# Optimization experiments

Hardware: AMD Instinct MI355X
Metric: run time of the kernel (lower is better)

The kernel has to match this reference:

```python
import jax, jax.numpy as jnp
import numpy as np

RRELU_SLOPE = (1.0 / 8.0 + 1.0 / 3.0) / 2.0  # F.rrelu eval-mode slope
DILATIONS = (1, 2, 4, 8)
HIDDEN_TEMP = 1.0
GUMBEL_TEMP = 0.1


def rrelu(x):
    return jnp.where(x >= 0, x, RRELU_SLOPE * x)


def conv1d(x, w, b, dilation):
    # x: [B, Cin, T], w: [Cout, Cin, K] -> [B, Cout, T'] (VALID, dilated)
    y = jax.lax.conv_general_dilated(
        x, w, window_strides=(1,), padding='VALID', rhs_dilation=(dilation,),
        dimension_numbers=('NCH', 'OIH', 'NCH'))
    return y + b[None, :, None]


def setup_inputs() -> dict:
    key = jax.random.key(0)
    ks = jax.random.split(key, 16)
    B, D, T, R = 8, 32, 4096, 8
    s = 0.05  # param scale for numerical stability
    inp = {
        'x': jax.random.normal(ks[0], (B, D, T), jnp.float32),
        'u': jax.random.uniform(ks[1], (B, T, R), jnp.float32, 1e-6, 1.0 - 1e-6),
        'conv_w0': jax.random.normal(ks[2], (128, D, 2), jnp.float32) * s,
        'conv_b0': jax.random.normal(ks[3], (128,), jnp.float32) * s,
        'conv_w1': jax.random.normal(ks[4], (128, 128, 2), jnp.float32) * s,
        'conv_b1': jax.random.normal(ks[5], (128,), jnp.float32) * s,
        'conv_w2': jax.random.normal(ks[6], (128, 128, 2), jnp.float32) * s,
        'conv_b2': jax.random.normal(ks[7], (128,), jnp.float32) * s,
        'conv_w3': jax.random.normal(ks[8], (R, 128, 2), jnp.float32) * s,
        'conv_b3': jax.random.normal(ks[9], (R,), jnp.float32) * s,
        'pw0': jax.random.normal(ks[10], (R, 256, 128), jnp.float32) * s,
        'pb0': jax.random.normal(ks[11], (R, 256), jnp.float32) * s,
        'pw1': jax.random.normal(ks[12], (R, 2 * D, 256), jnp.float32) * s,
        'pb1': jax.random.normal(ks[13], (R, 2 * D), jnp.float32) * s,
    }
    return inp


def reference(x, u, conv_w0, conv_b0, conv_w1, conv_b1, conv_w2, conv_b2,
              conv_w3, conv_b3, pw0, pb0, pw1, pb1):
    pad = sum(DILATIONS)  # causal left pad
    h = jnp.pad(x, ((0, 0), (0, 0), (pad, 0)))
    for w, b, d in ((conv_w0, conv_b0, DILATIONS[0]),
                    (conv_w1, conv_b1, DILATIONS[1]),
                    (conv_w2, conv_b2, DILATIONS[2])):
        h = rrelu(conv1d(h, w, b, d))
    pre = h  # [B, 128, T + dilations[-1]]
    h_vecs = rrelu(conv1d(pre, conv_w3, conv_b3, DILATIONS[3]))  # [B, R, T]
    pre = pre[:, :, DILATIONS[3]:]  # [B, 128, T]

    p = jax.nn.softmax(h_vecs / HIDDEN_TEMP, axis=1)  # [B, R, T]
    logits = jnp.log(p).transpose(0, 2, 1)  # [B, T, R]
    g = -jnp.log(-jnp.log(u))  # gumbel noise from uniform input
    gen_z = jax.nn.softmax((logits + g) / GUMBEL_TEMP, axis=-1).transpose(0, 2, 1)  # [B, R, T]

    # Fused mixture-of-experts dynamic linear: equal to materializing
    # einsum('brt,roi->boit') then contracting with pre, but avoids the huge tensor.
    params = (jnp.einsum('brt,roi,bit->bot', gen_z, pw0, pre)
              + jnp.einsum('brt,ro->bot', gen_z, pb0))
    # NOTE: original calls F.rrelu(params) without assignment -> no-op (kept faithful)
    params = (jnp.einsum('brt,roi,bit->bot', gen_z, pw1, params)
              + jnp.einsum('brt,ro->bot', gen_z, pb1))

    mus, sig = jnp.split(params, 2, axis=1)  # each [B, n_dims, T]
    sigmas = 0.5 + 0.5 * jnp.tanh(sig) + 0.001
    return mus, sigmas, gen_z
```

## Files before the change

### kernel.cpp

```cpp
#include <hip/hip_runtime.h>
#include <math.h>

typedef __attribute__((ext_vector_type(8))) short bf16x8;
typedef __attribute__((ext_vector_type(4))) float f32x4;
struct __align__(8)  us4 { unsigned short x,y,z,w; };
struct __align__(16) ui4 { unsigned x,y,z,w; };

#define SLOPE 0.2291666666666667f
constexpr int N0=4110, N1=4108, N2=4104, NX=4111;

__device__ __forceinline__ unsigned short f2bf(float f){
  unsigned u = __float_as_uint(f);
  u = (u + 0x7FFF + ((u>>16)&1)) >> 16;
  return (unsigned short)u;
}
__device__ __forceinline__ float bf2f(unsigned short h){
  return __uint_as_float(((unsigned)h)<<16);
}
__device__ __forceinline__ float rrelu(float v){ return v>=0.f ? v : v*SLOPE; }

__global__ __launch_bounds__(256) void prep_w(
  const float* __restrict__ w0, const float* __restrict__ w1, const float* __restrict__ w2,
  const float* __restrict__ pw0, const float* __restrict__ pw1,
  const float* __restrict__ pb0, const float* __restrict__ pb1,
  unsigned short* __restrict__ w0e, unsigned short* __restrict__ w1e, unsigned short* __restrict__ w2e,
  unsigned short* __restrict__ pw0b, unsigned short* __restrict__ pw1b,
  unsigned short* __restrict__ pb0e, unsigned short* __restrict__ pb1e)
{
  int idx = blockIdx.x*256 + threadIdx.x;
  if (idx < 8192){ int oc=idx>>6, k=idx&63, tap=k>>5, i=k&31;
    w0e[idx] = f2bf(w0[(oc*32+i)*2+tap]); return; }
  idx -= 8192;
  if (idx < 32768){ int oc=idx>>8, k=idx&255, tap=k>>7, i=k&127;
    w1e[idx] = f2bf(w1[(oc*128+i)*2+tap]); return; }
  idx -= 32768;
  if (idx < 32768){ int oc=idx>>8, k=idx&255, tap=k>>7, i=k&127;
    w2e[idx] = f2bf(w2[(oc*128+i)*2+tap]); return; }
  idx -= 32768;
  if (idx < 262144){ pw0b[idx] = f2bf(pw0[idx]); return; }
  idx -= 262144;
  if (idx < 131072){ pw1b[idx] = f2bf(pw1[idx]); return; }
  idx -= 131072;
  if (idx < 8192){ int o=idx>>5, r=idx&31; pb0e[idx] = r<8 ? f2bf(pb0[r*256+o]) : (unsigned short)0; return; }
  idx -= 8192;
  if (idx < 2048){ int o=idx>>5, r=idx&31; pb1e[idx] = r<8 ? f2bf(pb1[r*64+o]) : (unsigned short)0; return; }
}

__global__ __launch_bounds__(64) void prep_xt(const float* __restrict__ x,
                                              unsigned short* __restrict__ xt)
{
  __shared__ float s[32][64];
  const int b = blockIdx.y, j0 = blockIdx.x*64, l = threadIdx.x;
  #pragma unroll 4
  for (int i=0;i<32;i++){
    int p = j0 + l - 15;
    s[i][l] = (p>=0 && p<4096) ? x[((size_t)b*32+i)*4096+p] : 0.f;
  }
  __syncthreads();
  const int j = j0 + l;
  if (j < NX){
    unsigned tmp[16];
    #pragma unroll
    for (int q=0;q<16;q++)
      tmp[q] = (unsigned)f2bf(s[2*q][l]) | ((unsigned)f2bf(s[2*q+1][l])<<16);
    ui4* dst = (ui4*)(xt + ((size_t)b*NX + j)*32);
    #pragma unroll
    for (int q=0;q<4;q++){ ui4 v={tmp[4*q],tmp[4*q+1],tmp[4*q+2],tmp[4*q+3]}; dst[q]=v; }
  }
}

template<int IC, int DIL, int NIN, int NOUT>
__global__ __launch_bounds__(256) void conv_g(
    const unsigned short* __restrict__ act,
    const unsigned short* __restrict__ wgt,
    const float* __restrict__ bias,
    unsigned short* __restrict__ outp)
{
  constexpr int KT   = 2*IC;
  constexpr int NK   = KT/32;
  constexpr int NH   = (KT > 128) ? 2 : 1;
  constexpr int KPH  = KT / NH;
  constexpr int NKH  = KPH/32;
  constexpr int HRB  = KPH*2;
  constexpr int HCPR = HRB/16;
  __shared__ __align__(16) char wsm[64*HRB];
  __shared__ __align__(16) char outs[64*128];

  const int tid = threadIdx.x;
  const int b = blockIdx.z, ob = blockIdx.y, tb = blockIdx.x*64;
  const int o0g = ob*64;
  const int wid = tid>>6, l = tid&63, lo = l&15, hi = l>>4;

  bf16x8 bfr[NK];
  {
    const int tg = tb + wid*16 + lo;
    const int te = tg < NOUT ? tg : NOUT-1;
    #pragma unroll
    for (int kk=0;kk<NK;kk++){
      int k = kk*32 + hi*8;
      int tap = (k >= IC) ? 1 : 0;
      int off = k - tap*IC;
      bfr[kk] = *(const bf16x8*)(act + ((size_t)b*NIN + te + tap*DIL)*IC + off);
    }
  }

  f32x4 acc[4];
  #pragma unroll
  for (int m=0;m<4;m++) acc[m] = (f32x4){0.f,0.f,0.f,0.f};

  #pragma unroll
  for (int h=0; h<NH; ++h){
    __syncthreads();
    for (int c = tid; c < 64*HCPR; c += 256){
      int row = c / HCPR, cc = c % HCPR;
      ui4 v = *(const ui4*)((const char*)wgt + (size_t)(o0g+row)*KT*2 + h*HRB + cc*16);
      *(ui4*)(wsm + row*HRB + ((cc*16) ^ ((row&7)<<4))) = v;
    }
    __syncthreads();
    #pragma unroll
    for (int kk=0;kk<NKH;kk++){
      #pragma unroll
      for (int m=0;m<4;m++){
        int row = m*16 + lo;
        bf16x8 af = *(const bf16x8*)(wsm + row*HRB + ((kk*64+hi*16) ^ ((row&7)<<4)));
        acc[m] = __builtin_amdgcn_mfma_f32_16x16x32_bf16(af, bfr[h*NKH+kk], acc[m], 0,0,0);
      }
    }
  }
  __syncthreads();
  #pragma unroll
  for (int m=0;m<4;m++){
    const int ol = m*16 + hi*4;
    float b0v = bias[o0g+ol+0], b1v = bias[o0g+ol+1], b2v = bias[o0g+ol+2], b3v = bias[o0g+ol+3];
    int tl = wid*16 + lo;
    us4 v;
    v.x = f2bf(rrelu(acc[m][0] + b0v));
    v.y = f2bf(rrelu(acc[m][1] + b1v));
    v.z = f2bf(rrelu(acc[m][2] + b2v));
    v.w = f2bf(rrelu(acc[m][3] + b3v));
    *(us4*)(outs + tl*128 + ((ol*2) ^ ((tl&7)<<4))) = v;
  }
  __syncthreads();
  #pragma unroll
  for (int i=0;i<2;i++){
    int c = tid + i*256;
    int row = c>>3, cc = c&7;
    if (tb + row < NOUT){
      ui4 v = *(const ui4*)(outs + row*128 + ((cc*16) ^ ((row&7)<<4)));
      *(ui4*)(outp + ((size_t)b*NOUT + tb + row)*128 + o0g + cc*8) = v;
    }
  }
}

__global__ __launch_bounds__(64) void gumbel_g(
  const unsigned short* __restrict__ h2t,
  const float* __restrict__ w3, const float* __restrict__ b3,
  const float* __restrict__ u,
  float* __restrict__ genz,
  unsigned short* __restrict__ zt)
{
  __shared__ unsigned hs[72][66];
  const int b = blockIdx.y, t0 = blockIdx.x*64, l = threadIdx.x;
  const unsigned* src = (const unsigned*)(h2t + ((size_t)b*N2 + t0)*128);
  for (int e=l; e<72*64; e+=64) hs[e>>6][e&63] = src[e];
  __syncthreads();

  float acc[8];
  #pragma unroll
  for (int r=0;r<8;r++) acc[r]=b3[r];
  for (int i2=0;i2<64;i2++){
    unsigned a0 = hs[l][i2], a1 = hs[l+8][i2];
    float v00 = bf2f(a0&0xffff), v01 = bf2f(a0>>16);
    float v10 = bf2f(a1&0xffff), v11 = bf2f(a1>>16);
    const int i = 2*i2;
    #pragma unroll
    for (int r=0;r<8;r++){
      acc[r] = fmaf(w3[(r*128+i)*2],     v00, acc[r]);
      acc[r] = fmaf(w3[(r*128+i)*2+1],   v10, acc[r]);
      acc[r] = fmaf(w3[(r*128+i+1)*2],   v01, acc[r]);
      acc[r] = fmaf(w3[(r*128+i+1)*2+1], v11, acc[r]);
    }
  }
  float m = -1e30f;
  #pragma unroll
  for (int r=0;r<8;r++){ acc[r] = rrelu(acc[r]); m = fmaxf(m, acc[r]); }
  float s = 0.f;
  #pragma unroll
  for (int r=0;r<8;r++) s += __expf(acc[r]-m);
  const float lse = m + __logf(s);
  const int t = t0 + l;
  const float* ub = u + ((size_t)b*4096 + t)*8;
  float y[8], m2 = -1e30f;
  #pragma unroll
  for (int r=0;r<8;r++){
    float g = -__logf(-__logf(ub[r]));
    y[r] = (acc[r] - lse + g)*10.f;
    m2 = fmaxf(m2, y[r]);
  }
  float s2 = 0.f;
  #pragma unroll
  for (int r=0;r<8;r++){ y[r] = __expf(y[r]-m2); s2 += y[r]; }
  const float inv = 1.f/s2;
  #pragma unroll
  for (int r=0;r<8;r++){
    y[r] *= inv;
    genz[((size_t)b*8+r)*4096 + t] = y[r];
  }
  ui4 zp = { (unsigned)f2bf(y[0]) | ((unsigned)f2bf(y[1])<<16),
             (unsigned)f2bf(y[2]) | ((unsigned)f2bf(y[3])<<16),
             (unsigned)f2bf(y[4]) | ((unsigned)f2bf(y[5])<<16),
             (unsigned)f2bf(y[6]) | ((unsigned)f2bf(y[7])<<16) };
  ui4 zz = {0,0,0,0};
  ui4* zd = (ui4*)(zt + ((size_t)b*4096 + t)*32);
  zd[0]=zp; zd[1]=zz; zd[2]=zz; zd[3]=zz;
}

__global__ __launch_bounds__(256) void moe1_m(
  const unsigned short* __restrict__ h2t,
  const float* __restrict__ genz,
  const unsigned short* __restrict__ zt,
  const unsigned short* __restrict__ pw0b,
  const unsigned short* __restrict__ pb0e,
  unsigned short* __restrict__ hidt)
{
  __shared__ __align__(16) char pres[32768];
  __shared__ __align__(16) char outb[16384];
  __shared__ float zl[1024];

  const int ob = blockIdx.x, b = blockIdx.z, tb = blockIdx.y*128;
  const int o0g = ob*64;
  const int tid = threadIdx.x;
  #pragma unroll
  for (int i=0;i<4;i++){
    int e = tid + i*256;
    zl[e] = genz[((size_t)b*8 + (e>>7))*4096 + tb + (e&127)];
  }
  {
    const char* src = (const char*)(h2t + ((size_t)b*N2 + tb + 8)*128);
    #pragma unroll
    for (int i=0;i<8;i++){
      int c = tid + i*256, row = c>>4, cc = c&15;
      ui4 v = *(const ui4*)(src + row*256 + cc*16);
      *(ui4*)(pres + row*256 + ((cc*16) ^ ((row&7)<<4))) = v;
    }
  }
  __syncthreads();

  const int wid = tid>>6, l = tid&63, lo = l&15, hi = l>>4;
  const int ow = o0g + wid*16;

  f32x4 acc[8];
  {
    bf16x8 pf = *(const bf16x8*)(pb0e + (size_t)(ow + lo)*32 + hi*8);
    #pragma unroll
    for (int n=0;n<8;n++){
      bf16x8 zf = *(const bf16x8*)(zt + ((size_t)b*4096 + tb + n*16 + lo)*32 + hi*8);
      acc[n] = __builtin_amdgcn_mfma_f32_16x16x32_bf16(pf, zf, (f32x4){0.f,0.f,0.f,0.f}, 0,0,0);
    }
  }

  const unsigned short* abase = pw0b + (size_t)(ow + lo)*128 + hi*8;
  bf16x8 A[4], An[4];
  #pragma unroll
  for (int kk=0;kk<4;kk++) A[kk] = *(const bf16x8*)(abase + kk*32);

  #pragma unroll
  for (int r=0;r<8;r++){
    if (r < 7){
      #pragma unroll
      for (int kk=0;kk<4;kk++)
        An[kk] = *(const bf16x8*)(abase + (size_t)(r+1)*32768 + kk*32);
    }
    f32x4 ar[8];
    #pragma unroll
    for (int n=0;n<8;n++) ar[n] = (f32x4){0.f,0.f,0.f,0.f};
    #pragma unroll
    for (int kk=0;kk<4;kk++){
      #pragma unroll
      for (int n=0;n<8;n++){
        int tl = n*16 + lo;
        bf16x8 bf = *(const bf16x8*)(pres + tl*256 + ((kk*64 + hi*16) ^ ((tl&7)<<4)));
        ar[n] = __builtin_amdgcn_mfma_f32_16x16x32_bf16(A[kk], bf, ar[n], 0,0,0);
      }
    }
    #pragma unroll
    for (int n=0;n<8;n++){
      float zv = zl[r*128 + n*16 + lo];
      #pragma unroll
      for (int c2=0;c2<4;c2++)
        acc[n][c2] = fmaf(zv, ar[n][c2], acc[n][c2]);
    }
    if (r < 7){
      #pragma unroll
      for (int kk=0;kk<4;kk++) A[kk] = An[kk];
    }
  }

  #pragma unroll
  for (int n=0;n<8;n++){
    int tl = n*16 + lo;
    int ol2 = (wid*16 + hi*4)*2;
    us4 v;
    v.x=f2bf(acc[n][0]); v.y=f2bf(acc[n][1]); v.z=f2bf(acc[n][2]); v.w=f2bf(acc[n][3]);
    *(us4*)(outb + tl*128 + (ol2 ^ ((tl&7)<<4))) = v;
  }
  __syncthreads();
  #pragma unroll
  for (int i=0;i<4;i++){
    int c = tid + i*256, row = c>>3, cc = c&7;
    ui4 v = *(const ui4*)(outb + row*128 + ((cc*16) ^ ((row&7)<<4)));
    *(ui4*)(hidt + (((size_t)b*4 + ob)*4096 + tb + row)*64 + cc*8) = v;
  }
}

__global__ __launch_bounds__(512) void moe2_m(
  const unsigned short* __restrict__ hidt,
  const float* __restrict__ genz,
  const unsigned short* __restrict__ zt,
  const unsigned short* __restrict__ pw1b,
  const unsigned short* __restrict__ pb1e,
  float* __restrict__ out)
{
  __shared__ __align__(16) char smem[32768*2 + 4096];
  char* abuf0 = smem;
  char* abuf1 = smem + 32768;
  float* zl  = (float*)(smem + 65536);

  const int wg = blockIdx.x;
  const int b = wg >> 5, tb = (wg & 31) * 128;

  const int tid = threadIdx.x;
  #pragma unroll
  for (int i=0;i<2;i++){
    int e = tid + i*512;
    zl[e] = genz[((size_t)b*8 + (e>>7))*4096 + tb + (e&127)];
  }

  const int wid = tid>>6, l = tid&63, lo = l&15, hi = l>>4;
  const int tg = tb + wid*16 + lo;

  bf16x8 bfr[8];
  #pragma unroll
  for (int kk=0;kk<8;kk++)
    bfr[kk] = *(const bf16x8*)(hidt + (((size_t)b*4 + (kk>>1))*4096 + tg)*64 + (kk&1)*32 + hi*8);
  f32x4 acc[4];
  {
    bf16x8 zf = *(const bf16x8*)(zt + ((size_t)b*4096 + tg)*32 + hi*8);
    #pragma unroll
    for (int m=0;m<4;m++){
      bf16x8 pf = *(const bf16x8*)(pb1e + (size_t)(m*16 + lo)*32 + hi*8);
      acc[m] = __builtin_amdgcn_mfma_f32_16x16x32_bf16(pf, zf, (f32x4){0.f,0.f,0.f,0.f}, 0,0,0);
    }
  }

  {
    const char* src = (const char*)pw1b;
    #pragma unroll
    for (int i=0;i<4;i++){
      int c = tid + i*512, row = c>>5, cc = c&31;
      ui4 v = *(const ui4*)(src + row*512 + cc*16);
      *(ui4*)(abuf0 + row*512 + ((cc*16) ^ ((row&7)<<4))) = v;
    }
  }
  __syncthreads();

  #pragma unroll
  for (int r=0;r<8;r++){
    char* cur = (r&1) ? abuf1 : abuf0;
    char* nxt = (r&1) ? abuf0 : abuf1;
    ui4 stg[4];
    if (r < 7){
      const char* src = (const char*)(pw1b + (size_t)(r+1)*16384);
      #pragma unroll
      for (int i=0;i<4;i++){
        int c = tid + i*512;
        stg[i] = *(const ui4*)(src + (c>>5)*512 + (c&31)*16);
      }
    }
    f32x4 ar[4];
    #pragma unroll
    for (int m=0;m<4;m++) ar[m] = (f32x4){0.f,0.f,0.f,0.f};
    #pragma unroll
    for (int kk=0;kk<8;kk++){
      #pragma unroll
      for (int m=0;m<4;m++){
        int row = m*16 + lo;
        int kb  = kk*64 + hi*16;
        bf16x8 af = *(const bf16x8*)(cur + row*512 + (kb ^ ((row&7)<<4)));
        ar[m] = __builtin_amdgcn_mfma_f32_16x16x32_bf16(af, bfr[kk], ar[m], 0,0,0);
      }
    }
    float zv = zl[r*128 + wid*16 + lo];
    #pragma unroll
    for (int m=0;m<4;m++)
      #pragma unroll
      for (int c2=0;c2<4;c2++)
        acc[m][c2] = fmaf(zv, ar[m][c2], acc[m][c2]);
    if (r < 7){
      #pragma unroll
      for (int i=0;i<4;i++){
        int c = tid + i*512;
        *(ui4*)(nxt + (c>>5)*512 + (((c&31)*16) ^ (((c>>5)&7)<<4))) = stg[i];
      }
    }
    __syncthreads();
  }

  #pragma unroll
  for (int m=0;m<4;m++){
    #pragma unroll
    for (int c2=0;c2<4;c2++){
      int o = m*16 + hi*4 + c2;
      float v = acc[m][c2];
      if (o < 32)
        out[((size_t)b*32 + o)*4096 + tg] = v;
      else {
        float e = __expf(2.f*v);
        float th = 1.f - 2.f/(e+1.f);
        out[(size_t)1048576 + ((size_t)b*32 + (o-32))*4096 + tg] = 0.5f + 0.5f*th + 0.001f;
      }
    }
  }
}

extern "C" void kernel_launch(void* const* d_in, const int* in_sizes, int n_in,
                              void* d_out, int out_size, void* d_ws, size_t ws_size,
                              hipStream_t stream) {
  const float* x   = (const float*)d_in[0];
  const float* u   = (const float*)d_in[1];
  const float* w0  = (const float*)d_in[2];
  const float* b0  = (const float*)d_in[3];
  const float* w1  = (const float*)d_in[4];
  const float* b1  = (const float*)d_in[5];
  const float* w2  = (const float*)d_in[6];
  const float* b2  = (const float*)d_in[7];
  const float* w3  = (const float*)d_in[8];
  const float* b3  = (const float*)d_in[9];
  const float* pw0 = (const float*)d_in[10];
  const float* pb0 = (const float*)d_in[11];
  const float* pw1 = (const float*)d_in[12];
  const float* pb1 = (const float*)d_in[13];

  float* out  = (float*)d_out;
  float* genz = out + (size_t)2*8*32*4096;

  char* p = (char*)d_ws;
  unsigned short* xt   = (unsigned short*)p; p += 2104832;
  unsigned short* h0t  = (unsigned short*)p; p += 8417280;
  unsigned short* h1t  = (unsigned short*)p; p += 8413184;
  unsigned short* h2t  = (unsigned short*)p; p += 8404992;
  unsigned short* ztb  = (unsigned short*)p; p += 2097152;
  unsigned short* hidt = (unsigned short*)p; p += 16777216;
  unsigned short* w0e  = (unsigned short*)p; p += 16384;
  unsigned short* w1e  = (unsigned short*)p; p += 65536;
  unsigned short* w2e  = (unsigned short*)p; p += 65536;
  unsigned short* pw0b = (unsigned short*)p; p += 524288;
  unsigned short* pw1b = (unsigned short*)p; p += 262144;
  unsigned short* pb0e = (unsigned short*)p; p += 16384;
  unsigned short* pb1e = (unsigned short*)p; p += 4096;

  prep_w<<<1864, 256, 0, stream>>>(w0,w1,w2,pw0,pw1,pb0,pb1,
                                   w0e,w1e,w2e,pw0b,pw1b,pb0e,pb1e);
  prep_xt<<<dim3(65,8), 64, 0, stream>>>(x, xt);
  conv_g<32,1,NX,N0><<<dim3(65,2,8), 256, 0, stream>>>(xt,  w0e, b0, h0t);
  conv_g<128,2,N0,N1><<<dim3(65,2,8), 256, 0, stream>>>(h0t, w1e, b1, h1t);
  conv_g<128,4,N1,N2><<<dim3(65,2,8), 256, 0, stream>>>(h1t, w2e, b2, h2t);
  gumbel_g<<<dim3(64,8), 64, 0, stream>>>(h2t, w3, b3, u, genz, ztb);
  moe1_m<<<dim3(4,32,8), 256, 0, stream>>>(h2t, genz, ztb, pw0b, pb0e, hidt);
  moe2_m<<<256, 512, 0, stream>>>(hidt, genz, ztb, pw1b, pb1e, out);
}
```

Baseline: 127.7 us.

## Restructure dilated conv: stage activations in LDS, compute all 128 outputs per block

The conv kernel now has each block compute all 128 output channels for a 64-timestep tile, instead of splitting outputs across two blocks. The activation tile, including the dilation halo, is staged once into swizzled LDS, and weights are read straight from global into registers. This removes the duplicated activation loads across output-channel blocks and the per-half weight staging syncs. In exchange it halves the grid to 520 blocks, which may underfill the GPU, and leans on cached global weight reads.

```diff
diff --git a/kernel.cpp b/kernel.cpp
--- a/kernel.cpp
+++ b/kernel.cpp
@@ -78,76 +78,76 @@
 {
   constexpr int KT   = 2*IC;
   constexpr int NK   = KT/32;
-  constexpr int NH   = (KT > 128) ? 2 : 1;
-  constexpr int KPH  = KT / NH;
-  constexpr int NKH  = KPH/32;
-  constexpr int HRB  = KPH*2;
-  constexpr int HCPR = HRB/16;
-  __shared__ __align__(16) char wsm[64*HRB];
-  __shared__ __align__(16) char outs[64*128];
+  constexpr int ICB  = IC*2;
+  constexpr int ACPR = ICB/16;
+  constexpr int AR   = 64 + DIL;
+  constexpr int ASW  = (ICB>=256) ? 7 : 3;
+  __shared__ __align__(16) char acts[AR*ICB];
+  __shared__ __align__(16) char outs[64*256];
 
   const int tid = threadIdx.x;
-  const int b = blockIdx.z, ob = blockIdx.y, tb = blockIdx.x*64;
-  const int o0g = ob*64;
+  const int b = blockIdx.y, tb = blockIdx.x*64;
+
+  {
+    const char* ab = (const char*)(act + (size_t)b*NIN*IC);
+    for (int c = tid; c < AR*ACPR; c += 256){
+      int row = c / ACPR, cc = c % ACPR;
+      int tg = tb + row; if (tg > NIN-1) tg = NIN-1;
+      ui4 v = *(const ui4*)(ab + (size_t)tg*ICB + cc*16);
+      *(ui4*)(acts + row*ICB + ((cc*16) ^ ((row&ASW)<<4))) = v;
+    }
+  }
+  __syncthreads();
+
   const int wid = tid>>6, l = tid&63, lo = l&15, hi = l>>4;
-
-  bf16x8 bfr[NK];
-  {
-    const int tg = tb + wid*16 + lo;
-    const int te = tg < NOUT ? tg : NOUT-1;
-    #pragma unroll
-    for (int kk=0;kk<NK;kk++){
-      int k = kk*32 + hi*8;
-      int tap = (k >= IC) ? 1 : 0;
-      int off = k - tap*IC;
-      bfr[kk] = *(const bf16x8*)(act + ((size_t)b*NIN + te + tap*DIL)*IC + off);
-    }
-  }
-
-  f32x4 acc[4];
-  #pragma unroll
-  for (int m=0;m<4;m++) acc[m] = (f32x4){0.f,0.f,0.f,0.f};
-
-  #pragma unroll
-  for (int h=0; h<NH; ++h){
-    __syncthreads();
-    for (int c = tid; c < 64*HCPR; c += 256){
-      int row = c / HCPR, cc = c % HCPR;
-      ui4 v = *(const ui4*)((const char*)wgt + (size_t)(o0g+row)*KT*2 + h*HRB + cc*16);
-      *(ui4*)(wsm + row*HRB + ((cc*16) ^ ((row&7)<<4))) = v;
-    }
-    __syncthreads();
-    #pragma unroll
-    for (int kk=0;kk<NKH;kk++){
-      #pragma unroll
-      for (int m=0;m<4;m++){
-        int row = m*16 + lo;
-        bf16x8 af = *(const bf16x8*)(wsm + row*HRB + ((kk*64+hi*16) ^ ((row&7)<<4)));
-        acc[m] = __builtin_amdgcn_mfma_f32_16x16x32_bf16(af, bfr[h*NKH+kk], acc[m], 0,0,0);
-      }
-    }
-  }
-  __syncthreads();
-  #pragma unroll
-  for (int m=0;m<4;m++){
-    const int ol = m*16 + hi*4;
-    float b0v = bias[o0g+ol+0], b1v = bias[o0g+ol+1], b2v = bias[o0g+ol+2], b3v = bias[o0g+ol+3];
-    int tl = wid*16 + lo;
-    us4 v;
-    v.x = f2bf(rrelu(acc[m][0] + b0v));
-    v.y = f2bf(rrelu(acc[m][1] + b1v));
-    v.z = f2bf(rrelu(acc[m][2] + b2v));
-    v.w = f2bf(rrelu(acc[m][3] + b3v));
-    *(us4*)(outs + tl*128 + ((ol*2) ^ ((tl&7)<<4))) = v;
-  }
-  __syncthreads();
-  #pragma unroll
-  for (int i=0;i<2;i++){
+  const int ow = wid*32;
+
+  f32x4 acc[2][4];
+  #pragma unroll
+  for (int m=0;m<2;m++)
+    #pragma unroll
+    for (int n=0;n<4;n++) acc[m][n] = (f32x4){0.f,0.f,0.f,0.f};
+
+  const unsigned short* abase = wgt + (size_t)(ow + lo)*KT + hi*8;
+  #pragma unroll
+  for (int kk=0;kk<NK;kk++){
+    bf16x8 A0 = *(const bf16x8*)(abase + kk*32);
+    bf16x8 A1 = *(const bf16x8*)(abase + 16*KT + kk*32);
+    const int k = kk*32 + hi*8;
+    const int tap = (k >= IC) ? 1 : 0;
+    const int off2 = (k - tap*IC)*2;
+    #pragma unroll
+    for (int n=0;n<4;n++){
+      int arow = n*16 + lo + tap*DIL;
+      bf16x8 bf = *(const bf16x8*)(acts + arow*ICB + (off2 ^ ((arow&ASW)<<4)));
+      acc[0][n] = __builtin_amdgcn_mfma_f32_16x16x32_bf16(A0, bf, acc[0][n], 0,0,0);
+      acc[1][n] = __builtin_amdgcn_mfma_f32_16x16x32_bf16(A1, bf, acc[1][n], 0,0,0);
+    }
+  }
+
+  #pragma unroll
+  for (int m=0;m<2;m++){
+    const int ol = ow + m*16 + hi*4;
+    float b0v = bias[ol+0], b1v = bias[ol+1], b2v = bias[ol+2], b3v = bias[ol+3];
+    #pragma unroll
+    for (int n=0;n<4;n++){
+      int tl = n*16 + lo;
+      us4 v;
+      v.x = f2bf(rrelu(acc[m][n][0] + b0v));
+      v.y = f2bf(rrelu(acc[m][n][1] + b1v));
+      v.z = f2bf(rrelu(acc[m][n][2] + b2v));
+      v.w = f2bf(rrelu(acc[m][n][3] + b3v));
+      *(us4*)(outs + tl*256 + ((ol*2) ^ ((tl&7)<<4))) = v;
+    }
+  }
+  __syncthreads();
+  #pragma unroll
+  for (int i=0;i<4;i++){
     int c = tid + i*256;
-    int row = c>>3, cc = c&7;
+    int row = c>>4, cc = c&15;
     if (tb + row < NOUT){
-      ui4 v = *(const ui4*)(outs + row*128 + ((cc*16) ^ ((row&7)<<4)));
-      *(ui4*)(outp + ((size_t)b*NOUT + tb + row)*128 + o0g + cc*8) = v;
+      ui4 v = *(const ui4*)(outs + row*256 + ((cc*16) ^ ((row&7)<<4)));
+      *(ui4*)(outp + ((size_t)b*NOUT + tb + row)*128 + cc*8) = v;
     }
   }
 }
@@ -462,9 +462,9 @@
   prep_w<<<1864, 256, 0, stream>>>(w0,w1,w2,pw0,pw1,pb0,pb1,
                                    w0e,w1e,w2e,pw0b,pw1b,pb0e,pb1e);
   prep_xt<<<dim3(65,8), 64, 0, stream>>>(x, xt);
-  conv_g<32,1,NX,N0><<<dim3(65,2,8), 256, 0, stream>>>(xt,  w0e, b0, h0t);
-  conv_g<128,2,N0,N1><<<dim3(65,2,8), 256, 0, stream>>>(h0t, w1e, b1, h1t);
-  conv_g<128,4,N1,N2><<<dim3(65,2,8), 256, 0, stream>>>(h1t, w2e, b2, h2t);
+  conv_g<32,1,NX,N0><<<dim3(65,8), 256, 0, stream>>>(xt,  w0e, b0, h0t);
+  conv_g<128,2,N0,N1><<<dim3(65,8), 256, 0, stream>>>(h0t, w1e, b1, h1t);
+  conv_g<128,4,N1,N2><<<dim3(65,8), 256, 0, stream>>>(h1t, w2e, b2, h2t);
   gumbel_g<<<dim3(64,8), 64, 0, stream>>>(h2t, w3, b3, u, genz, ztb);
   moe1_m<<<dim3(4,32,8), 256, 0, stream>>>(h2t, genz, ztb, pw0b, pb0e, hidt);
   moe2_m<<<256, 512, 0, stream>>>(hidt, genz, ztb, pw1b, pb1e, out);
```

Result: no change. 127.6 us (-0.1%).
